# Optimization experiments

Measured on AMD Instinct MI355X. Metric: run time of the kernel, lower is better.

## Reference

```python
import jax, jax.numpy as jnp
import numpy as np

B, S, D = 4, 16, 512          # batch, seq, attention_dim
V, T = 32000, 18              # vocab_size, tree_depth
INNER = V - 1                 # internal nodes of Huffman tree


def setup_inputs() -> dict:
    key = jax.random.key(0)
    k_att, k_w, k_idx, k_bit = jax.random.split(key, 4)
    att = jax.random.normal(k_att, (B, S, D), dtype=jnp.float32)
    weight = jax.random.normal(k_w, (INNER, D), dtype=jnp.float32) * 0.02
    path_index = jax.random.randint(k_idx, (V * T,), 0, INNER, dtype=jnp.int64)
    # left/right branch bits: sign=+1,bias=0 -> p ; sign=-1,bias=1 -> 1-p
    bits = jax.random.randint(k_bit, (V * T,), 0, 2).astype(jnp.float32)
    path_sign = 1.0 - 2.0 * bits
    path_bias = bits
    return {
        "att": att,
        "weight": weight,
        "path_index": path_index,
        "path_sign": path_sign,
        "path_bias": path_bias,
        "vocab_size": V,
        "tree_depth": T,
    }


def reference(att, weight, path_index, path_sign, path_bias, vocab_size, tree_depth):
    # h: sigmoid of linear projection onto internal-node vectors  [B,S,INNER]
    h = jax.nn.sigmoid(jnp.einsum("bsd,nd->bsn", att, weight))
    # gather per-(token,depth) internal-node probs, flip via sign/bias
    g = jnp.take(h, path_index, axis=-1) * path_sign + path_bias  # [B,S,V*T]
    Hm = g.reshape(att.shape[0], -1, vocab_size, tree_depth)      # [B,S,V,T]
    return jnp.sum(jnp.log(Hm), axis=-1)                          # [B,S,V]
```

## Files before the change

kernel.cpp:

```cpp
#include <hip/hip_runtime.h>
#include <hip/hip_bf16.h>

#define BS    64
#define DDIM  512
#define NV    32000
#define TD    18
#define INNER 31999
#define ROWP  32000

typedef __attribute__((ext_vector_type(8))) short short8;
typedef __attribute__((ext_vector_type(4))) float floatx4;

__device__ __forceinline__ float bf16_to_f32(unsigned short u) {
    union { unsigned int i; float f; } v; v.i = ((unsigned int)u) << 16; return v.f;
}
__device__ __forceinline__ unsigned short f32_to_bf16(float f) {
    union { float f; unsigned int i; } v; v.f = f;
    unsigned int r = v.i + 0x7FFFu + ((v.i >> 16) & 1u);
    return (unsigned short)(r >> 16);
}

#define IDXB 2250
__global__ __launch_bounds__(256) void prep(
    const int* __restrict__ idx,
    const unsigned int* __restrict__ signbits,
    unsigned short* __restrict__ idx2T,
    const float4* __restrict__ att,
    ushort4* __restrict__ attb)
{
    const int b = blockIdx.x;
    if (b < IDXB) {
        const unsigned int* w = (const unsigned int*)idx;
        bool i64 = true;
#pragma unroll
        for (int j = 1; j < 16; j += 2) i64 &= (w[j] == 0u);
        int o = b * 256 + threadIdx.x;
        int t = o / NV, v = o - t * NV;
        int i = v * TD + t;
        int val = i64 ? idx[2 * i] : idx[i];
        idx2T[o] = (unsigned short)((val << 1) | (int)(signbits[i] >> 31));
    } else {
        int i = (b - IDXB) * 256 + threadIdx.x;
        float4 a = att[i];
        ushort4 r;
        r.x = f32_to_bf16(a.x); r.y = f32_to_bf16(a.y);
        r.z = f32_to_bf16(a.z); r.w = f32_to_bf16(a.w);
        attb[i] = r;
    }
}

__global__ __launch_bounds__(256) void gemm_logsig(
    const unsigned short* __restrict__ attb,
    const float* __restrict__ weight,
    unsigned int* __restrict__ pairs)
{
    const int lane = threadIdx.x & 63;
    const int wave = threadIdx.x >> 6;
    const int nb   = blockIdx.x * 64 + wave * 16;
    const int l15  = lane & 15;
    const int quad = lane >> 4;

    floatx4 acc[4];
#pragma unroll
    for (int i = 0; i < 4; ++i) acc[i] = (floatx4){0.f, 0.f, 0.f, 0.f};

    int brow = nb + l15;
    if (brow > INNER - 1) brow = INNER - 1;
    const float*          bbase = weight + (size_t)brow * DDIM + quad * 8;
    const unsigned short* abase = attb + l15 * DDIM + quad * 8;

#pragma unroll 4
    for (int k0 = 0; k0 < DDIM; k0 += 32) {
        float4 b0 = *(const float4*)(bbase + k0);
        float4 b1 = *(const float4*)(bbase + k0 + 4);
        short8 bfrag;
        bfrag[0] = (short)f32_to_bf16(b0.x); bfrag[1] = (short)f32_to_bf16(b0.y);
        bfrag[2] = (short)f32_to_bf16(b0.z); bfrag[3] = (short)f32_to_bf16(b0.w);
        bfrag[4] = (short)f32_to_bf16(b1.x); bfrag[5] = (short)f32_to_bf16(b1.y);
        bfrag[6] = (short)f32_to_bf16(b1.z); bfrag[7] = (short)f32_to_bf16(b1.w);
#pragma unroll
        for (int mt = 0; mt < 4; ++mt) {
            short8 afrag = *(const short8*)(abase + mt * 16 * DDIM + k0);
            acc[mt] = __builtin_amdgcn_mfma_f32_16x16x32_bf16(afrag, bfrag, acc[mt], 0, 0, 0);
        }
    }

    const int n = nb + l15;
    if (n < INNER) {
#pragma unroll
        for (int mt = 0; mt < 4; ++mt) {
#pragma unroll
            for (int r = 0; r < 4; ++r) {
                const int m = mt * 16 + quad * 4 + r;
                float x = acc[mt][r];
                float lp = -(fmaxf(-x, 0.f) + __logf(1.f + __expf(-fabsf(x))));
                float lm = lp - x;
                pairs[m * ROWP + n] = (unsigned int)f32_to_bf16(lp)
                                    | ((unsigned int)f32_to_bf16(lm) << 16);
            }
        }
    }
}

__global__ __launch_bounds__(1024) void gather_pairs(
    const unsigned int* __restrict__ pairs,
    const unsigned short* __restrict__ idx2T,
    float* __restrict__ out)
{
    extern __shared__ unsigned int lds32[];
    const int bs    = blockIdx.y;
    const int vbase = blockIdx.x * 8000;
    const int tid   = threadIdx.x;

    const uint4* src = (const uint4*)(pairs + (size_t)bs * ROWP);
    for (int i = tid; i < ROWP / 4; i += 1024) ((uint4*)lds32)[i] = src[i];
    __syncthreads();

#pragma unroll
    for (int s = 0; s < 8; ++s) {
        int r = s * 1024 + tid;
        if (r < 8000) {
            const unsigned short* col = idx2T + vbase + r;
            float sum = 0.f;
#pragma unroll
            for (int t = 0; t < TD; ++t) {
                unsigned int e = col[(size_t)t * NV];
                unsigned int p = lds32[e >> 1];
                unsigned short h = (e & 1u) ? (unsigned short)(p >> 16)
                                            : (unsigned short)(p & 0xFFFFu);
                sum += bf16_to_f32(h);
            }
            out[bs * NV + vbase + r] = sum;
        }
    }
}

extern "C" void kernel_launch(void* const* d_in, const int* in_sizes, int n_in,
                              void* d_out, int out_size, void* d_ws, size_t ws_size,
                              hipStream_t stream)
{
    const float*        att    = (const float*)d_in[0];
    const float*        weight = (const float*)d_in[1];
    const int*          pidx   = (const int*)d_in[2];
    const unsigned int* psign  = (const unsigned int*)d_in[3];
    float* out = (float*)d_out;

    char* ws = (char*)d_ws;
    unsigned int*   pairs = (unsigned int*)ws;
    unsigned short* idx2T = (unsigned short*)(ws + 8192000);
    ushort4*        attb  = (ushort4*)       (ws + 9344000);

    hipFuncSetAttribute(reinterpret_cast<const void*>(gather_pairs),
                        hipFuncAttributeMaxDynamicSharedMemorySize, ROWP * 4);

    prep<<<IDXB + 32, 256, 0, stream>>>(pidx, psign, idx2T, (const float4*)att, attb);
    gemm_logsig<<<500, 256, 0, stream>>>((const unsigned short*)attb, weight, pairs);
    gather_pairs<<<dim3(4, BS), 1024, ROWP * 4, stream>>>(pairs, idx2T, out);
}
```

Baseline: 145.0 us.

## Fuse prep, GEMM and gather into one cooperative kernel with grid syncs

Replaces the three separate launches (index/att prep, bf16 MFMA GEMM with log-sigmoid, LDS gather-sum) with one cooperative kernel of 256 blocks of 1024 threads. The stages are separated by grid.sync(). The aim is to remove launch gaps and inter-kernel drain between stages. In exchange the GEMM stage runs on fewer blocks, with 16 waves per block each taking a tile, and the gather stage maps one block per (bs, quarter). The 128KB LDS request limits the kernel to one block per CU, and the old three-kernel path is kept as a fallback if the cooperative launch fails.

```diff
diff --git a/kernel.cpp b/kernel.cpp
--- a/kernel.cpp
+++ b/kernel.cpp
@@ -1,5 +1,8 @@
 #include <hip/hip_runtime.h>
 #include <hip/hip_bf16.h>
+#include <hip/hip_cooperative_groups.h>
+
+namespace cg = cooperative_groups;
 
 #define BS    64
 #define DDIM  512
@@ -7,6 +10,7 @@
 #define TD    18
 #define INNER 31999
 #define ROWP  32000
+#define NTOT  576000
 
 typedef __attribute__((ext_vector_type(8))) short short8;
 typedef __attribute__((ext_vector_type(4))) float floatx4;
@@ -20,13 +24,128 @@
     return (unsigned short)(r >> 16);
 }
 
-#define IDXB 2250
-__global__ __launch_bounds__(256) void prep(
+__global__ __launch_bounds__(1024) void fused(
+    const float4* __restrict__ att4,
+    const float* __restrict__ weight,
     const int* __restrict__ idx,
     const unsigned int* __restrict__ signbits,
+    unsigned int* __restrict__ pairs,
     unsigned short* __restrict__ idx2T,
-    const float4* __restrict__ att,
-    ushort4* __restrict__ attb)
+    unsigned short* __restrict__ attb,
+    float* __restrict__ out)
+{
+    extern __shared__ unsigned int lds32[];
+    cg::grid_group grid = cg::this_grid();
+    const int blk = blockIdx.x;
+    const int tid = threadIdx.x;
+
+    {
+        const unsigned int* w = (const unsigned int*)idx;
+        bool i64 = true;
+#pragma unroll
+        for (int j = 1; j < 16; j += 2) i64 &= (w[j] == 0u);
+
+        for (int o = blk * 1024 + tid; o < NTOT; o += 256 * 1024) {
+            int t = o / NV, v = o - t * NV;
+            int i = v * TD + t;
+            int val = i64 ? idx[2 * i] : idx[i];
+            idx2T[o] = (unsigned short)((val << 1) | (int)(signbits[i] >> 31));
+        }
+        if (blk < 8) {
+            int i = blk * 1024 + tid;
+            float4 a = att4[i];
+            ushort4 r;
+            r.x = f32_to_bf16(a.x); r.y = f32_to_bf16(a.y);
+            r.z = f32_to_bf16(a.z); r.w = f32_to_bf16(a.w);
+            ((ushort4*)attb)[i] = r;
+        }
+    }
+    grid.sync();
+
+    {
+        const int wave = tid >> 6, lane = tid & 63;
+        const int tile = wave * 256 + blk;
+        if (tile < 2000) {
+            const int nb  = tile * 16;
+            const int l15 = lane & 15, quad = lane >> 4;
+
+            floatx4 acc[4];
+#pragma unroll
+            for (int i = 0; i < 4; ++i) acc[i] = (floatx4){0.f, 0.f, 0.f, 0.f};
+
+            int brow = nb + l15;
+            if (brow > INNER - 1) brow = INNER - 1;
+            const float*          bbase = weight + (size_t)brow * DDIM + quad * 8;
+            const unsigned short* abase = attb + l15 * DDIM + quad * 8;
+
+#pragma unroll 4
+            for (int k0 = 0; k0 < DDIM; k0 += 32) {
+                float4 b0 = *(const float4*)(bbase + k0);
+                float4 b1 = *(const float4*)(bbase + k0 + 4);
+                short8 bfrag;
+                bfrag[0] = (short)f32_to_bf16(b0.x); bfrag[1] = (short)f32_to_bf16(b0.y);
+                bfrag[2] = (short)f32_to_bf16(b0.z); bfrag[3] = (short)f32_to_bf16(b0.w);
+                bfrag[4] = (short)f32_to_bf16(b1.x); bfrag[5] = (short)f32_to_bf16(b1.y);
+                bfrag[6] = (short)f32_to_bf16(b1.z); bfrag[7] = (short)f32_to_bf16(b1.w);
+#pragma unroll
+                for (int mt = 0; mt < 4; ++mt) {
+                    short8 afrag = *(const short8*)(abase + mt * 16 * DDIM + k0);
+                    acc[mt] = __builtin_amdgcn_mfma_f32_16x16x32_bf16(afrag, bfrag, acc[mt], 0, 0, 0);
+                }
+            }
+
+            const int n = nb + l15;
+            if (n < INNER) {
+#pragma unroll
+                for (int mt = 0; mt < 4; ++mt) {
+#pragma unroll
+                    for (int r = 0; r < 4; ++r) {
+                        const int m = mt * 16 + quad * 4 + r;
+                        float x = acc[mt][r];
+                        float lp = -(fmaxf(-x, 0.f) + __logf(1.f + __expf(-fabsf(x))));
+                        float lm = lp - x;
+                        pairs[m * ROWP + n] = (unsigned int)f32_to_bf16(lp)
+                                            | ((unsigned int)f32_to_bf16(lm) << 16);
+                    }
+                }
+            }
+        }
+    }
+    grid.sync();
+
+    {
+        const int bs    = blk >> 2;
+        const int vbase = (blk & 3) * 8000;
+
+        const uint4* src = (const uint4*)(pairs + (size_t)bs * ROWP);
+        for (int i = tid; i < ROWP / 4; i += 1024) ((uint4*)lds32)[i] = src[i];
+        __syncthreads();
+
+#pragma unroll
+        for (int s = 0; s < 8; ++s) {
+            int r = s * 1024 + tid;
+            if (r < 8000) {
+                const unsigned short* col = idx2T + vbase + r;
+                float sum = 0.f;
+#pragma unroll
+                for (int t = 0; t < TD; ++t) {
+                    unsigned int e = col[(size_t)t * NV];
+                    unsigned int p = lds32[e >> 1];
+                    unsigned short h = (e & 1u) ? (unsigned short)(p >> 16)
+                                                : (unsigned short)(p & 0xFFFFu);
+                    sum += bf16_to_f32(h);
+                }
+                out[bs * NV + vbase + r] = sum;
+            }
+        }
+    }
+}
+
+#define IDXB 2250
+__global__ __launch_bounds__(256) void prep_fb(
+    const int* __restrict__ idx, const unsigned int* __restrict__ signbits,
+    unsigned short* __restrict__ idx2T,
+    const float4* __restrict__ att, ushort4* __restrict__ attb)
 {
     const int b = blockIdx.x;
     if (b < IDXB) {
@@ -49,9 +168,8 @@
     }
 }
 
-__global__ __launch_bounds__(256) void gemm_logsig(
-    const unsigned short* __restrict__ attb,
-    const float* __restrict__ weight,
+__global__ __launch_bounds__(256) void gemm_fb(
+    const unsigned short* __restrict__ attb, const float* __restrict__ weight,
     unsigned int* __restrict__ pairs)
 {
     const int lane = threadIdx.x & 63;
@@ -102,9 +220,8 @@
     }
 }
 
-__global__ __launch_bounds__(1024) void gather_pairs(
-    const unsigned int* __restrict__ pairs,
-    const unsigned short* __restrict__ idx2T,
+__global__ __launch_bounds__(1024) void gather_fb(
+    const unsigned int* __restrict__ pairs, const unsigned short* __restrict__ idx2T,
     float* __restrict__ out)
 {
     extern __shared__ unsigned int lds32[];
@@ -139,7 +256,7 @@
                               void* d_out, int out_size, void* d_ws, size_t ws_size,
                               hipStream_t stream)
 {
-    const float*        att    = (const float*)d_in[0];
+    const float4*       att4   = (const float4*)d_in[0];
     const float*        weight = (const float*)d_in[1];
     const int*          pidx   = (const int*)d_in[2];
     const unsigned int* psign  = (const unsigned int*)d_in[3];
@@ -148,12 +265,22 @@
     char* ws = (char*)d_ws;
     unsigned int*   pairs = (unsigned int*)ws;
     unsigned short* idx2T = (unsigned short*)(ws + 8192000);
-    ushort4*        attb  = (ushort4*)       (ws + 9344000);
-
-    hipFuncSetAttribute(reinterpret_cast<const void*>(gather_pairs),
+    unsigned short* attb  = (unsigned short*)(ws + 9344000);
+
+    hipFuncSetAttribute(reinterpret_cast<const void*>(fused),
                         hipFuncAttributeMaxDynamicSharedMemorySize, ROWP * 4);
-
-    prep<<<IDXB + 32, 256, 0, stream>>>(pidx, psign, idx2T, (const float4*)att, attb);
-    gemm_logsig<<<500, 256, 0, stream>>>((const unsigned short*)attb, weight, pairs);
-    gather_pairs<<<dim3(4, BS), 1024, ROWP * 4, stream>>>(pairs, idx2T, out);
-}
+    hipFuncSetAttribute(reinterpret_cast<const void*>(gather_fb),
+                        hipFuncAttributeMaxDynamicSharedMemorySize, ROWP * 4);
+
+    void* args[] = { (void*)&att4, (void*)&weight, (void*)&pidx, (void*)&psign,
+                     (void*)&pairs, (void*)&idx2T, (void*)&attb, (void*)&out };
+    hipError_t e = hipLaunchCooperativeKernel(
+        reinterpret_cast<void*>(fused), dim3(256), dim3(1024),
+        args, ROWP * 4, stream);
+
+    if (e != hipSuccess) {
+        prep_fb<<<IDXB + 32, 256, 0, stream>>>(pidx, psign, idx2T, att4, (ushort4*)attb);
+        gemm_fb<<<500, 256, 0, stream>>>(attb, weight, pairs);
+        gather_fb<<<dim3(4, BS), 1024, ROWP * 4, stream>>>(pairs, idx2T, out);
+    }
+}
```

Measured after the change: 234.4 us. 1.62x slower.

## Transpose pair table to node-major and gather per-vocab with lanes over tokens

Applied to the files above, without the earlier changes.

The GEMM epilogue now writes the log-sigmoid pairs in node-major layout (64 tokens contiguous per node) using vector stores. The gather kernel maps each wave lane to one of the 64 (batch,seq) rows and reads path indices as wave-uniform scalars, so each tree-node lookup becomes a coalesced 256-byte global read. This replaces the per-row LDS staging of the whole 128KB table, and the index prep no longer transposes. The cost is reliance on L2 for random node rows, and output stores are strided by NV per lane.

```diff
diff --git a/kernel.cpp b/kernel.cpp
--- a/kernel.cpp
+++ b/kernel.cpp
@@ -6,7 +6,7 @@
 #define NV    32000
 #define TD    18
 #define INNER 31999
-#define ROWP  32000
+#define NPAD  32000
 
 typedef __attribute__((ext_vector_type(8))) short short8;
 typedef __attribute__((ext_vector_type(4))) float floatx4;
@@ -24,7 +24,7 @@
 __global__ __launch_bounds__(256) void prep(
     const int* __restrict__ idx,
     const unsigned int* __restrict__ signbits,
-    unsigned short* __restrict__ idx2T,
+    unsigned short* __restrict__ idx2,
     const float4* __restrict__ att,
     ushort4* __restrict__ attb)
 {
@@ -34,11 +34,9 @@
         bool i64 = true;
 #pragma unroll
         for (int j = 1; j < 16; j += 2) i64 &= (w[j] == 0u);
-        int o = b * 256 + threadIdx.x;
-        int t = o / NV, v = o - t * NV;
-        int i = v * TD + t;
+        int i = b * 256 + threadIdx.x;
         int val = i64 ? idx[2 * i] : idx[i];
-        idx2T[o] = (unsigned short)((val << 1) | (int)(signbits[i] >> 31));
+        idx2[i] = (unsigned short)((val << 1) | (int)(signbits[i] >> 31));
     } else {
         int i = (b - IDXB) * 256 + threadIdx.x;
         float4 a = att[i];
@@ -52,7 +50,7 @@
 __global__ __launch_bounds__(256) void gemm_logsig(
     const unsigned short* __restrict__ attb,
     const float* __restrict__ weight,
-    unsigned int* __restrict__ pairs)
+    unsigned int* __restrict__ pairsT)
 {
     const int lane = threadIdx.x & 63;
     const int wave = threadIdx.x >> 6;
@@ -87,51 +85,53 @@
 
     const int n = nb + l15;
     if (n < INNER) {
+        unsigned int* dst = pairsT + (size_t)n * 64 + quad * 4;
 #pragma unroll
         for (int mt = 0; mt < 4; ++mt) {
+            uint4 pk;
 #pragma unroll
             for (int r = 0; r < 4; ++r) {
-                const int m = mt * 16 + quad * 4 + r;
                 float x = acc[mt][r];
                 float lp = -(fmaxf(-x, 0.f) + __logf(1.f + __expf(-fabsf(x))));
                 float lm = lp - x;
-                pairs[m * ROWP + n] = (unsigned int)f32_to_bf16(lp)
-                                    | ((unsigned int)f32_to_bf16(lm) << 16);
+                ((unsigned int*)&pk)[r] = (unsigned int)f32_to_bf16(lp)
+                                        | ((unsigned int)f32_to_bf16(lm) << 16);
             }
+            *(uint4*)(dst + mt * 16) = pk;
         }
     }
 }
 
-__global__ __launch_bounds__(1024) void gather_pairs(
-    const unsigned int* __restrict__ pairs,
-    const unsigned short* __restrict__ idx2T,
+__global__ __launch_bounds__(256) void gather_T(
+    const unsigned int* __restrict__ pairsT,
+    const unsigned short* __restrict__ idx2,
     float* __restrict__ out)
 {
-    extern __shared__ unsigned int lds32[];
-    const int bs    = blockIdx.y;
-    const int vbase = blockIdx.x * 8000;
-    const int tid   = threadIdx.x;
-
-    const uint4* src = (const uint4*)(pairs + (size_t)bs * ROWP);
-    for (int i = tid; i < ROWP / 4; i += 1024) ((uint4*)lds32)[i] = src[i];
-    __syncthreads();
+    const int lane = threadIdx.x & 63;
+    const int wave = threadIdx.x >> 6;
 
 #pragma unroll
-    for (int s = 0; s < 8; ++s) {
-        int r = s * 1024 + tid;
-        if (r < 8000) {
-            const unsigned short* col = idx2T + vbase + r;
-            float sum = 0.f;
+    for (int g = 0; g < 4; ++g) {
+        const int v0 = blockIdx.x * 64 + wave * 16 + g * 4;
+        const unsigned short* ip = idx2 + (size_t)v0 * TD;
+        float a0 = 0.f, a1 = 0.f, a2 = 0.f, a3 = 0.f;
 #pragma unroll
-            for (int t = 0; t < TD; ++t) {
-                unsigned int e = col[(size_t)t * NV];
-                unsigned int p = lds32[e >> 1];
-                unsigned short h = (e & 1u) ? (unsigned short)(p >> 16)
-                                            : (unsigned short)(p & 0xFFFFu);
-                sum += bf16_to_f32(h);
-            }
-            out[bs * NV + vbase + r] = sum;
+        for (int t = 0; t < TD; ++t) {
+            unsigned int e0 = __builtin_amdgcn_readfirstlane(ip[t]);
+            unsigned int e1 = __builtin_amdgcn_readfirstlane(ip[TD + t]);
+            unsigned int e2 = __builtin_amdgcn_readfirstlane(ip[2 * TD + t]);
+            unsigned int e3 = __builtin_amdgcn_readfirstlane(ip[3 * TD + t]);
+            unsigned int p0 = pairsT[(size_t)(e0 >> 1) * 64 + lane];
+            unsigned int p1 = pairsT[(size_t)(e1 >> 1) * 64 + lane];
+            unsigned int p2 = pairsT[(size_t)(e2 >> 1) * 64 + lane];
+            unsigned int p3 = pairsT[(size_t)(e3 >> 1) * 64 + lane];
+            a0 += bf16_to_f32((e0 & 1u) ? (unsigned short)(p0 >> 16) : (unsigned short)(p0 & 0xFFFFu));
+            a1 += bf16_to_f32((e1 & 1u) ? (unsigned short)(p1 >> 16) : (unsigned short)(p1 & 0xFFFFu));
+            a2 += bf16_to_f32((e2 & 1u) ? (unsigned short)(p2 >> 16) : (unsigned short)(p2 & 0xFFFFu));
+            a3 += bf16_to_f32((e3 & 1u) ? (unsigned short)(p3 >> 16) : (unsigned short)(p3 & 0xFFFFu));
         }
+        float4 st = {a0, a1, a2, a3};
+        *(float4*)(out + (size_t)lane * NV + v0) = st;
     }
 }
 
@@ -139,21 +139,18 @@
                               void* d_out, int out_size, void* d_ws, size_t ws_size,
                               hipStream_t stream)
 {
-    const float*        att    = (const float*)d_in[0];
+    const float4*       att4   = (const float4*)d_in[0];
     const float*        weight = (const float*)d_in[1];
     const int*          pidx   = (const int*)d_in[2];
     const unsigned int* psign  = (const unsigned int*)d_in[3];
     float* out = (float*)d_out;
 
     char* ws = (char*)d_ws;
-    unsigned int*   pairs = (unsigned int*)ws;
-    unsigned short* idx2T = (unsigned short*)(ws + 8192000);
-    ushort4*        attb  = (ushort4*)       (ws + 9344000);
+    unsigned int*   pairsT = (unsigned int*)ws;
+    unsigned short* idx2   = (unsigned short*)(ws + 8192000);
+    unsigned short* attb   = (unsigned short*)(ws + 9344000);
 
-    hipFuncSetAttribute(reinterpret_cast<const void*>(gather_pairs),
-                        hipFuncAttributeMaxDynamicSharedMemorySize, ROWP * 4);
-
-    prep<<<IDXB + 32, 256, 0, stream>>>(pidx, psign, idx2T, (const float4*)att, attb);
-    gemm_logsig<<<500, 256, 0, stream>>>((const unsigned short*)attb, weight, pairs);
-    gather_pairs<<<dim3(4, BS), 1024, ROWP * 4, stream>>>(pairs, idx2T, out);
+    prep<<<IDXB + 32, 256, 0, stream>>>(pidx, psign, idx2, att4, (ushort4*)attb);
+    gemm_logsig<<<500, 256, 0, stream>>>(attb, weight, pairsT);
+    gather_T<<<500, 256, 0, stream>>>(pairsT, idx2, out);
 }
```

Measured after the change: 145.2 us. No clear change (+0.1%).
